# Kernel tuning notes

Measured on AMD Instinct MI355X. Metric: run time of the kernel, lower is better.

## Reference

```python
import jax, jax.numpy as jnp
import numpy as np


def setup_inputs() -> dict:
    key = jax.random.key(0)
    kx, kb, kc, ka, kd = jax.random.split(key, 5)
    B, L, D, N = 8, 4096, 1024, 128
    x = jax.random.normal(kx, (B, L, D), jnp.float32)
    B_w = jax.random.normal(kb, (N, D), jnp.float32) * 0.01  # nn.Linear(d_model->d_state).weight
    C_w = jax.random.normal(kc, (D, N), jnp.float32)         # nn.Linear(d_state->d_model).weight
    # stable negative log_A (HiPPO init gives -|diag|+0.1 < 0)
    log_A = -jax.random.uniform(ka, (N,), jnp.float32) * 3.0 - 0.1
    D_param = jax.random.normal(kd, (D,), jnp.float32)
    return dict(x=x, B_w=B_w, C_w=C_w, log_A=log_A, D_param=D_param)


def reference(x, B_w, C_w, log_A, D_param):
    # x: (B,L,D); B_w: (N,D); C_w: (D,N); log_A: (N,); D_param: (D,)
    A = jnp.exp(log_A)                                   # (N,) diagonal transition
    x_proj = jnp.einsum('bld,nd->bln', x, B_w)           # B @ x  -> (B,L,N)

    def step(h, u):                                      # h_t = A*h_{t-1} + u_t
        h = A * h + u
        return h, h

    h0 = jnp.zeros((x.shape[0], B_w.shape[0]), x.dtype)  # (B,N)
    _, hs = jax.lax.scan(step, h0, jnp.swapaxes(x_proj, 0, 1))  # hs: (L,B,N)

    y = jnp.einsum('lbn,dn->bld', hs, C_w)               # C @ h -> (B,L,D)
    y = y + x * D_param                                  # skip term D*x

    last = x_proj[:, -1, :]                              # (B,N)
    final_state = jnp.broadcast_to(last.mean(axis=0, keepdims=True), last.shape)
    return y, final_state
```

## Files before the change

### kernel.cpp

```cpp
#include <hip/hip_runtime.h>


typedef _Float16 half8 __attribute__((ext_vector_type(8)));
typedef _Float16 half4 __attribute__((ext_vector_type(4)));
typedef float f32x4 __attribute__((ext_vector_type(4)));

#define BDIM 8
#define LDIM 4096
#define DDIM 1024
#define NDIM 128
#define MTOT (BDIM * LDIM)
#define CHUNK 32
#define NCHUNK (LDIM / CHUNK)
#define TOTCHUNK (BDIM * NCHUNK)

__device__ __forceinline__ void dma16(const void* g, void* l) {
    __builtin_amdgcn_global_load_lds((const __attribute__((address_space(1))) void*)g,
                                     (__attribute__((address_space(3))) void*)l, 16, 0, 0);
}

__global__ __launch_bounds__(256) void prep(const float* __restrict__ x,
                                            const float* __restrict__ Bw,
                                            const float* __restrict__ Cw,
                                            _Float16* __restrict__ Bwh,
                                            _Float16* __restrict__ Cwh,
                                            float* __restrict__ out) {
    const int blk = blockIdx.x;
    const int t = threadIdx.x;
    if (blk < 128) {
        const int n = blk;
        float s = 0.f;
        const float* br = Bw + n * DDIM;
        for (int b = 0; b < BDIM; ++b) {
            const float* xr = x + ((size_t)b * LDIM + (LDIM - 1)) * DDIM;
            for (int k = t; k < DDIM; k += 256)
                s = fmaf(xr[k], br[k], s);
        }
        __shared__ float red[256];
        red[t] = s;
        __syncthreads();
        for (int off = 128; off > 0; off >>= 1) {
            if (t < off) red[t] += red[t + off];
            __syncthreads();
        }
        if (t == 0) {
            float v = red[0] * 0.125f;
            for (int b = 0; b < BDIM; ++b)
                out[(size_t)MTOT * DDIM + b * NDIM + n] = v;
        }
    } else {
        const int base = (blk - 128) * 4096;
#pragma unroll
        for (int j = 0; j < 4; ++j) {
            int e = base + j * 1024 + t * 4;
            const float* src;
            _Float16* dst;
            if (e < 131072) { src = Bw + e; dst = Bwh + e; }
            else            { src = Cw + (e - 131072); dst = Cwh + (e - 131072); }
            float4 v = *reinterpret_cast<const float4*>(src);
            half4 h = { (_Float16)v.x, (_Float16)v.y, (_Float16)v.z, (_Float16)v.w };
            *reinterpret_cast<half4*>(dst) = h;
        }
    }
}

__global__ __launch_bounds__(256, 4) void gemm1(const float* __restrict__ x,
                                                const _Float16* __restrict__ Bwh,
                                                float* __restrict__ xp) {
    __shared__ _Float16 As[32 * 64];
    __shared__ _Float16 Bs[128 * 64];
    const int t = threadIdx.x;
    const int row0 = blockIdx.x * 32;
    const int wave = t >> 6, lane = t & 63;
    const int wr = (wave >> 1) * 16, wc = (wave & 1) * 64;
    const int lrow = lane & 15, kq = (lane >> 4) * 8;
    const int kc = kq >> 3;

    f32x4 acc[4] = {};

    for (int kk = 0; kk < DDIM; kk += 64) {
#pragma unroll
        for (int inst = 0; inst < 4; ++inst) {
            int s = inst * 256 + t;
            int r = s >> 3;
            int cs = (s & 7) ^ (r & 7);
            dma16(&Bwh[(size_t)r * DDIM + kk + cs * 8], &Bs[(inst * 256 + wave * 64) * 8]);
        }
#pragma unroll
        for (int j = 0; j < 2; ++j) {
            int s = t + 256 * j;
            int r = s >> 4, c4 = s & 15;
            float4 v = *reinterpret_cast<const float4*>(&x[(size_t)(row0 + r) * DDIM + kk + c4 * 4]);
            half4 h = { (_Float16)v.x, (_Float16)v.y, (_Float16)v.z, (_Float16)v.w };
            int pc = (c4 >> 1) ^ (r & 7);
            *reinterpret_cast<half4*>(&As[r * 64 + pc * 8 + (c4 & 1) * 4]) = h;
        }
        __syncthreads();

        half8 af[2], bf[2][4];
        const int arow = wr + lrow;
#pragma unroll
        for (int ks = 0; ks < 2; ++ks) {
            af[ks] = *reinterpret_cast<const half8*>(&As[arow * 64 + ((ks * 4 + kc) ^ (arow & 7)) * 8]);
#pragma unroll
            for (int ct = 0; ct < 4; ++ct) {
                int brow = wc + ct * 16 + lrow;
                bf[ks][ct] = *reinterpret_cast<const half8*>(&Bs[brow * 64 + ((ks * 4 + kc) ^ (brow & 7)) * 8]);
            }
        }
#pragma unroll
        for (int ks = 0; ks < 2; ++ks)
#pragma unroll
            for (int ct = 0; ct < 4; ++ct)
                acc[ct] = __builtin_amdgcn_mfma_f32_16x16x32_f16(af[ks], bf[ks][ct], acc[ct], 0, 0, 0);
        __syncthreads();
    }

    const int q4 = (lane >> 4) * 4;
#pragma unroll
    for (int ct = 0; ct < 4; ++ct) {
        int col = wc + ct * 16 + lrow;
#pragma unroll
        for (int i = 0; i < 4; ++i)
            xp[(row0 + wr + q4 + i) * NDIM + col] = acc[ct][i];
    }
}

__global__ void scan_agg(const float* __restrict__ xp, const float* __restrict__ logA,
                         float* __restrict__ agg) {
    const int chunk = blockIdx.x;
    const int n = threadIdx.x;
    const float A = expf(logA[n]);
    const float* u = xp + (size_t)chunk * CHUNK * NDIM + n;
    float h = 0.f;
#pragma unroll
    for (int j = 0; j < CHUNK; ++j)
        h = fmaf(A, h, u[j * NDIM]);
    agg[chunk * NDIM + n] = h;
}

__global__ void scan_carry(const float* __restrict__ agg, const float* __restrict__ logA,
                           float* __restrict__ hprev) {
    const int idx = blockIdx.x * blockDim.x + threadIdx.x;
    const int b = idx >> 7, n = idx & 127;
    const float Ac = expf((float)CHUNK * logA[n]);
    float c = 0.f;
    for (int ch = 0; ch < NCHUNK; ++ch) {
        int g = (b * NCHUNK + ch) * NDIM + n;
        hprev[g] = c;
        c = fmaf(Ac, c, agg[g]);
    }
}

__global__ void scan_final(const float* __restrict__ xp, const float* __restrict__ logA,
                           const float* __restrict__ hprev, _Float16* __restrict__ hs) {
    const int chunk = blockIdx.x;
    const int n = threadIdx.x;
    const float A = expf(logA[n]);
    float h = hprev[chunk * NDIM + n];
    const float* u = xp + (size_t)chunk * CHUNK * NDIM + n;
    _Float16* o = hs + (size_t)chunk * CHUNK * NDIM + n;
#pragma unroll
    for (int j = 0; j < CHUNK; ++j) {
        h = fmaf(A, h, u[j * NDIM]);
        o[j * NDIM] = (_Float16)h;
    }
}

#define BUFW 132
__global__ __launch_bounds__(256, 4) void gemm2(const _Float16* __restrict__ hs,
                                                const _Float16* __restrict__ Cwh,
                                                const float* __restrict__ x,
                                                const float* __restrict__ Dp,
                                                float* __restrict__ y) {
    __shared__ float buf[64 * BUFW];
    __shared__ __align__(16) float DpS[128];

    const int t = threadIdx.x;
    const int row0 = blockIdx.x * 128;
    const int col0 = blockIdx.y * 128;
    const int wave = t >> 6, lane = t & 63;
    const int wr = (wave >> 1) * 64, wc = (wave & 1) * 64;
    const int lrow = lane & 15, kq = (lane >> 4) * 8;

    if (t < 128) DpS[t] = Dp[col0 + t];

    const _Float16* ha = hs + (size_t)(row0 + wr + lrow) * NDIM + kq;
    const _Float16* cb = Cwh + (size_t)(col0 + wc + lrow) * NDIM + kq;

    f32x4 acc[4][4] = {};
#pragma unroll
    for (int kb = 0; kb < 4; ++kb) {
        half8 bf[4], af[4];
#pragma unroll
        for (int ct = 0; ct < 4; ++ct)
            bf[ct] = *reinterpret_cast<const half8*>(cb + (size_t)ct * 16 * NDIM + kb * 32);
#pragma unroll
        for (int rt = 0; rt < 4; ++rt)
            af[rt] = *reinterpret_cast<const half8*>(ha + (size_t)rt * 16 * NDIM + kb * 32);
#pragma unroll
        for (int rt = 0; rt < 4; ++rt)
#pragma unroll
            for (int ct = 0; ct < 4; ++ct)
                acc[rt][ct] = __builtin_amdgcn_mfma_f32_16x16x32_f16(af[rt], bf[ct], acc[rt][ct], 0, 0, 0);
    }

    const int q4 = (lane >> 4) * 4;
#pragma unroll
    for (int half_ = 0; half_ < 2; ++half_) {
        __syncthreads();
        if ((wr >> 6) == half_) {
#pragma unroll
            for (int rt = 0; rt < 4; ++rt)
#pragma unroll
                for (int ct = 0; ct < 4; ++ct) {
                    int col = wc + ct * 16 + lrow;
#pragma unroll
                    for (int i = 0; i < 4; ++i)
                        buf[(rt * 16 + q4 + i) * BUFW + col] = acc[rt][ct][i];
                }
        }
        __syncthreads();
#pragma unroll
        for (int j = 0; j < 8; ++j) {
            int idx = t + 256 * j;
            int row = idx >> 5, c4 = idx & 31;
            int grow = row0 + half_ * 64 + row;
            float4 a = *reinterpret_cast<const float4*>(&buf[row * BUFW + c4 * 4]);
            float4 xv = *reinterpret_cast<const float4*>(&x[(size_t)grow * DDIM + col0 + c4 * 4]);
            float4 dp = *reinterpret_cast<const float4*>(&DpS[c4 * 4]);
            float4 o;
            o.x = a.x + xv.x * dp.x;
            o.y = a.y + xv.y * dp.y;
            o.z = a.z + xv.z * dp.z;
            o.w = a.w + xv.w * dp.w;
            *reinterpret_cast<float4*>(&y[(size_t)grow * DDIM + col0 + c4 * 4]) = o;
        }
    }
}

extern "C" void kernel_launch(void* const* d_in, const int* in_sizes, int n_in,
                              void* d_out, int out_size, void* d_ws, size_t ws_size,
                              hipStream_t stream) {
    const float* x    = (const float*)d_in[0];
    const float* Bw   = (const float*)d_in[1];
    const float* Cw   = (const float*)d_in[2];
    const float* logA = (const float*)d_in[3];
    const float* Dp   = (const float*)d_in[4];
    float* out = (float*)d_out;

    char* ws = (char*)d_ws;
    float*    xp    = (float*)   (ws);
    _Float16* hs    = (_Float16*)(ws + 16777216);
    float*    agg   = (float*)   (ws + 25165824);
    float*    hprev = (float*)   (ws + 25690112);
    _Float16* Bwh   = (_Float16*)(ws + 26214400);
    _Float16* Cwh   = (_Float16*)(ws + 26476544);

    prep<<<192, 256, 0, stream>>>(x, Bw, Cw, Bwh, Cwh, out);
    gemm1<<<MTOT / 32, 256, 0, stream>>>(x, Bwh, xp);
    scan_agg<<<TOTCHUNK, 128, 0, stream>>>(xp, logA, agg);
    scan_carry<<<4, 256, 0, stream>>>(agg, logA, hprev);
    scan_final<<<TOTCHUNK, 128, 0, stream>>>(xp, logA, hprev, hs);
    gemm2<<<dim3(MTOT / 128, DDIM / 128), 256, 0, stream>>>(hs, Cwh, x, Dp, out);
}
```

Before: 343.6 us.

## Fuse chunk scan aggregation into gemm1 epilogue and stage hs via LDS in gemm2

```diff
diff --git a/kernel.cpp b/kernel.cpp
--- a/kernel.cpp
+++ b/kernel.cpp
@@ -64,9 +64,11 @@
     }
 }
 
-__global__ __launch_bounds__(256, 4) void gemm1(const float* __restrict__ x,
+__global__ __launch_bounds__(256, 8) void gemm1(const float* __restrict__ x,
                                                 const _Float16* __restrict__ Bwh,
-                                                float* __restrict__ xp) {
+                                                const float* __restrict__ logA,
+                                                float* __restrict__ xp,
+                                                float* __restrict__ agg) {
     __shared__ _Float16 As[32 * 64];
     __shared__ _Float16 Bs[128 * 64];
     const int t = threadIdx.x;
@@ -97,46 +99,48 @@
         }
         __syncthreads();
 
-        half8 af[2], bf[2][4];
         const int arow = wr + lrow;
 #pragma unroll
         for (int ks = 0; ks < 2; ++ks) {
-            af[ks] = *reinterpret_cast<const half8*>(&As[arow * 64 + ((ks * 4 + kc) ^ (arow & 7)) * 8]);
+            half8 af = *reinterpret_cast<const half8*>(&As[arow * 64 + ((ks * 4 + kc) ^ (arow & 7)) * 8]);
+            half8 bf[4];
 #pragma unroll
             for (int ct = 0; ct < 4; ++ct) {
                 int brow = wc + ct * 16 + lrow;
-                bf[ks][ct] = *reinterpret_cast<const half8*>(&Bs[brow * 64 + ((ks * 4 + kc) ^ (brow & 7)) * 8]);
+                bf[ct] = *reinterpret_cast<const half8*>(&Bs[brow * 64 + ((ks * 4 + kc) ^ (brow & 7)) * 8]);
             }
-        }
-#pragma unroll
-        for (int ks = 0; ks < 2; ++ks)
 #pragma unroll
             for (int ct = 0; ct < 4; ++ct)
-                acc[ct] = __builtin_amdgcn_mfma_f32_16x16x32_f16(af[ks], bf[ks][ct], acc[ct], 0, 0, 0);
-        __syncthreads();
-    }
-
+                acc[ct] = __builtin_amdgcn_mfma_f32_16x16x32_f16(af, bf[ct], acc[ct], 0, 0, 0);
+        }
+        __syncthreads();
+    }
+
+    float* tb = (float*)Bs;
     const int q4 = (lane >> 4) * 4;
 #pragma unroll
     for (int ct = 0; ct < 4; ++ct) {
         int col = wc + ct * 16 + lrow;
 #pragma unroll
         for (int i = 0; i < 4; ++i)
-            xp[(row0 + wr + q4 + i) * NDIM + col] = acc[ct][i];
-    }
-}
-
-__global__ void scan_agg(const float* __restrict__ xp, const float* __restrict__ logA,
-                         float* __restrict__ agg) {
-    const int chunk = blockIdx.x;
-    const int n = threadIdx.x;
-    const float A = expf(logA[n]);
-    const float* u = xp + (size_t)chunk * CHUNK * NDIM + n;
-    float h = 0.f;
-#pragma unroll
-    for (int j = 0; j < CHUNK; ++j)
-        h = fmaf(A, h, u[j * NDIM]);
-    agg[chunk * NDIM + n] = h;
+            tb[(wr + q4 + i) * NDIM + col] = acc[ct][i];
+    }
+    __syncthreads();
+#pragma unroll
+    for (int j = 0; j < 4; ++j) {
+        int idx = t + 256 * j;
+        int row = idx >> 5, c4 = idx & 31;
+        *reinterpret_cast<float4*>(&xp[(size_t)(row0 + row) * NDIM + c4 * 4]) =
+            *reinterpret_cast<const float4*>(&tb[row * NDIM + c4 * 4]);
+    }
+    if (t < 128) {
+        const float A = expf(logA[t]);
+        float h = 0.f;
+#pragma unroll
+        for (int j = 0; j < CHUNK; ++j)
+            h = fmaf(A, h, tb[j * NDIM + t]);
+        agg[(size_t)blockIdx.x * NDIM + t] = h;
+    }
 }
 
 __global__ void scan_carry(const float* __restrict__ agg, const float* __restrict__ logA,
@@ -145,6 +149,7 @@
     const int b = idx >> 7, n = idx & 127;
     const float Ac = expf((float)CHUNK * logA[n]);
     float c = 0.f;
+#pragma unroll 8
     for (int ch = 0; ch < NCHUNK; ++ch) {
         int g = (b * NCHUNK + ch) * NDIM + n;
         hprev[g] = c;
@@ -173,19 +178,31 @@
                                                 const float* __restrict__ x,
                                                 const float* __restrict__ Dp,
                                                 float* __restrict__ y) {
-    __shared__ float buf[64 * BUFW];
+    __shared__ __align__(16) char smem[64 * BUFW * 4];
     __shared__ __align__(16) float DpS[128];
+    _Float16* hsP = (_Float16*)smem;
 
     const int t = threadIdx.x;
-    const int row0 = blockIdx.x * 128;
-    const int col0 = blockIdx.y * 128;
+    const int id = blockIdx.x;
+    const int xb = (id & 7) * 32 + ((id >> 3) & 31);
+    const int yb = id >> 8;
+    const int row0 = xb * 128;
+    const int col0 = yb * 128;
     const int wave = t >> 6, lane = t & 63;
     const int wr = (wave >> 1) * 64, wc = (wave & 1) * 64;
     const int lrow = lane & 15, kq = (lane >> 4) * 8;
 
     if (t < 128) DpS[t] = Dp[col0 + t];
 
-    const _Float16* ha = hs + (size_t)(row0 + wr + lrow) * NDIM + kq;
+#pragma unroll
+    for (int inst = 0; inst < 8; ++inst) {
+        int s = inst * 256 + t;
+        int r = s >> 4, c = s & 15;
+        dma16(&hs[(size_t)(row0 + r) * NDIM + ((c ^ (r & 7)) * 8)],
+              &hsP[(inst * 256 + wave * 64) * 8]);
+    }
+    __syncthreads();
+
     const _Float16* cb = Cwh + (size_t)(col0 + wc + lrow) * NDIM + kq;
 
     f32x4 acc[4][4] = {};
@@ -196,8 +213,11 @@
         for (int ct = 0; ct < 4; ++ct)
             bf[ct] = *reinterpret_cast<const half8*>(cb + (size_t)ct * 16 * NDIM + kb * 32);
 #pragma unroll
-        for (int rt = 0; rt < 4; ++rt)
-            af[rt] = *reinterpret_cast<const half8*>(ha + (size_t)rt * 16 * NDIM + kb * 32);
+        for (int rt = 0; rt < 4; ++rt) {
+            int ar = wr + rt * 16 + lrow;
+            int ck = kb * 4 + (kq >> 3);
+            af[rt] = *reinterpret_cast<const half8*>(&hsP[ar * NDIM + ((ck ^ (ar & 7)) * 8)]);
+        }
 #pragma unroll
         for (int rt = 0; rt < 4; ++rt)
 #pragma unroll
@@ -205,6 +225,7 @@
                 acc[rt][ct] = __builtin_amdgcn_mfma_f32_16x16x32_f16(af[rt], bf[ct], acc[rt][ct], 0, 0, 0);
     }
 
+    float* buf = (float*)smem;
     const int q4 = (lane >> 4) * 4;
 #pragma unroll
     for (int half_ = 0; half_ < 2; ++half_) {
@@ -258,9 +279,8 @@
     _Float16* Cwh   = (_Float16*)(ws + 26476544);
 
     prep<<<192, 256, 0, stream>>>(x, Bw, Cw, Bwh, Cwh, out);
-    gemm1<<<MTOT / 32, 256, 0, stream>>>(x, Bwh, xp);
-    scan_agg<<<TOTCHUNK, 128, 0, stream>>>(xp, logA, agg);
-    scan_carry<<<4, 256, 0, stream>>>(agg, logA, hprev);
+    gemm1<<<MTOT / 32, 256, 0, stream>>>(x, Bwh, logA, xp, agg);
+    scan_carry<<<8, 128, 0, stream>>>(agg, logA, hprev);
     scan_final<<<TOTCHUNK, 128, 0, stream>>>(xp, logA, hprev, hs);
-    gemm2<<<dim3(MTOT / 128, DDIM / 128), 256, 0, stream>>>(hs, Cwh, x, Dp, out);
-}
+    gemm2<<<MTOT / 128 * (DDIM / 128), 256, 0, stream>>>(hs, Cwh, x, Dp, out);
+}
```

After: 341.6 us. No clear change (-0.6%).
